# Kernel tuning notes

Hardware: AMD Instinct MI355X
Metric: run time of the kernel (lower is better)

## Reference

```python
import jax, jax.numpy as jnp
import numpy as np

H = 12  # num_attention_heads


def setup_inputs() -> dict:
    key = jax.random.key(0)
    ks = jax.random.split(key, 7)
    B, T, L, D = 4, 64, 128, 768
    input_ids = jax.random.randint(ks[0], (B, T, L), 0, 30000, dtype=jnp.int32)
    speaker_ids = jax.random.randint(ks[1], (B, T), 0, 8, dtype=jnp.int32)
    token_embeddings = jax.random.normal(ks[2], (B, T, L, D), dtype=jnp.float32)
    edu_embeddings = jax.random.normal(ks[3], (B, T, D), dtype=jnp.float32)
    s = 1.0 / np.sqrt(D)
    Wk = jax.random.normal(ks[4], (D, D), dtype=jnp.float32) * s
    Wv = jax.random.normal(ks[5], (D, D), dtype=jnp.float32) * s
    Wq = jax.random.normal(ks[6], (D, D), dtype=jnp.float32) * s
    return {"input_ids": input_ids, "speaker_ids": speaker_ids,
            "token_embeddings": token_embeddings, "edu_embeddings": edu_embeddings,
            "Wk": Wk, "Wv": Wv, "Wq": Wq}


def reference(input_ids, speaker_ids, token_embeddings, edu_embeddings, Wk, Wv, Wq):
    B, T, L = input_ids.shape
    D = token_embeddings.shape[-1]
    d = D // H
    # per-turn keys/values, split into heads: [B,T,H,d]
    k = (edu_embeddings @ Wk.T).reshape(B, T, H, d)
    v = (edu_embeddings @ Wv.T).reshape(B, T, H, d)
    # per-head outer products k (x) v: [B,T,H,d,d]
    kv = jnp.einsum('bthd,bthe->bthde', k, v)
    # speaker-segmented inclusive prefix sum: M[b,t] = sum_{u<=t, spk[u]==spk[t]} kv[b,u]
    same = speaker_ids[:, None, :] == speaker_ids[:, :, None]        # [B,T(t),T(u)]
    causal = jnp.tril(jnp.ones((T, T), dtype=bool))                  # u <= t (inclusive)
    A = (same & causal).astype(kv.dtype)                             # [B,T,T]
    M = jnp.einsum('btu,buhde->bthde', A, kv)                        # [B,T,H,d,d]
    # token queries attend into their turn's speaker memory matrix
    q = (token_embeddings @ Wq.T).reshape(B, T, L, H, d)
    a = jnp.einsum('btlhd,bthde->btlhe', q, M).reshape(B, T, L, D)
    return token_embeddings + a
```

## Files before the change

### kernel.cpp

```cpp
#include <hip/hip_runtime.h>
#include <hip/hip_bf16.h>

#define NB 4
#define NT 64
#define NL 128
#define ND 768
#define NH 12
#define HD 64

typedef __attribute__((ext_vector_type(8))) short short8;
typedef __attribute__((ext_vector_type(4))) float f32x4;
typedef __attribute__((ext_vector_type(4))) unsigned int u32x4;

typedef __attribute__((address_space(3))) unsigned int lds_u32;
typedef __attribute__((address_space(1))) const unsigned int glob_u32;

static __device__ __forceinline__ unsigned short f2b(float x) {
    __hip_bfloat16 h = __float2bfloat16(x);
    return *reinterpret_cast<unsigned short*>(&h);
}
static __device__ __forceinline__ float b2f(unsigned short u) {
    unsigned int v = ((unsigned int)u) << 16;
    union { unsigned int i; float f; } c; c.i = v; return c.f;
}
static __device__ __forceinline__ void gl2lds16(const void* g, void* l) {
    __builtin_amdgcn_global_load_lds((glob_u32*)g, (lds_u32*)l, 16, 0, 0);
}
static __device__ __forceinline__ unsigned rne2(unsigned lo, unsigned hi) {
    lo += 0x7FFFu + ((lo >> 16) & 1u);
    hi += 0x7FFFu + ((hi >> 16) & 1u);
    return __builtin_amdgcn_perm(hi, lo, 0x07060302u);
}

#define TAIL_WQ4  147456u
#define TAIL_EDU4 196608u
#define TAIL_WK4  344064u
__global__ __launch_bounds__(256) void conv_bf16(
    const float* __restrict__ te, const float* __restrict__ Wq,
    const float* __restrict__ edu, const float* __restrict__ Wk,
    const float* __restrict__ Wv, unsigned short* __restrict__ dst)
{
    const unsigned tid = threadIdx.x;
    if (blockIdx.x < 3072u) {
        const unsigned base = blockIdx.x * 2048u + tid;
        u32x4 a[8];
        #pragma unroll
        for (int i = 0; i < 8; i++) {
            const u32x4* s = (const u32x4*)te + (base + i * 256u);
            a[i] = __builtin_nontemporal_load(s);
        }
        #pragma unroll
        for (int i = 0; i < 8; i++) {
            uint2 o;
            o.x = rne2(a[i].x, a[i].y);
            o.y = rne2(a[i].z, a[i].w);
            *(uint2*)(dst + (size_t)(base + i * 256u) * 4u) = o;
        }
    } else {
        const unsigned base = (blockIdx.x - 3072u) * 2048u + tid;
        u32x4 a[8];
        #pragma unroll
        for (int i = 0; i < 8; i++) {
            unsigned c = base + i * 256u;
            const float* s;
            if (c < TAIL_WQ4)       s = Wq  + (size_t)c * 4u;
            else if (c < TAIL_EDU4) s = edu + (size_t)(c - TAIL_WQ4)  * 4u;
            else if (c < TAIL_WK4)  s = Wk  + (size_t)(c - TAIL_EDU4) * 4u;
            else                    s = Wv  + (size_t)(c - TAIL_WK4)  * 4u;
            a[i] = *(const u32x4*)s;
        }
        unsigned short* d = dst + 25165824u;
        #pragma unroll
        for (int i = 0; i < 8; i++) {
            uint2 o;
            o.x = rne2(a[i].x, a[i].y);
            o.y = rne2(a[i].z, a[i].w);
            *(uint2*)(d + (size_t)(base + i * 256u) * 4u) = o;
        }
    }
}

__global__ __launch_bounds__(256) void kvm(
    const unsigned short* __restrict__ edu_b,
    const unsigned short* __restrict__ wk_b,
    const unsigned short* __restrict__ wv_b,
    const int* __restrict__ spk,
    unsigned short* __restrict__ Mt)
{
    const int h = blockIdx.x, b = blockIdx.y, eh = blockIdx.z;

    __shared__ float bucket[8][32][65];
    __shared__ float k_s[64][68];
    __shared__ float v_s[64][36];
    __shared__ __align__(16) unsigned short stage[10240];
    __shared__ int spk_s[64];
    unsigned short* edu_s = stage;
    unsigned short* wk_s  = stage + 4096;
    unsigned short* wv_s  = stage + 8192;

    const int tid = threadIdx.x, lane = tid & 63, wvx = tid >> 6;
    const int lr = lane & 15, lg = lane >> 4, r8 = lane >> 3, l8 = lane & 7;

    { float* p = &bucket[0][0][0];
      for (int i = tid; i < 8 * 32 * 65; i += 256) p[i] = 0.f; }
    if (tid < 64) spk_s[tid] = spk[b * NT + tid];

    const unsigned short* edub = edu_b + (size_t)(b * 64) * ND;
    const unsigned short* wkb  = wk_b + (size_t)(h * 64) * ND;
    const unsigned short* wvb  = wv_b + (size_t)(h * 64 + eh * 32) * ND;

    f32x4 acc_k[4], acc_v[2];
    #pragma unroll
    for (int i = 0; i < 4; i++) acc_k[i] = (f32x4){0.f, 0.f, 0.f, 0.f};
    #pragma unroll
    for (int i = 0; i < 2; i++) acc_v[i] = (f32x4){0.f, 0.f, 0.f, 0.f};

    const int sswz = ((l8 ^ r8) * 8);

    for (int k0 = 0; k0 < ND; k0 += 64) {
        __syncthreads();
        #pragma unroll
        for (int j = 0; j < 5; j++) {
            const int cid = wvx * 5 + j;
            const unsigned short* gs; unsigned short* ls;
            if (cid < 8)       { gs = edub + (size_t)(cid * 8 + r8) * ND;        ls = edu_s + cid * 512; }
            else if (cid < 16) { gs = wkb  + (size_t)((cid - 8) * 8 + r8) * ND;  ls = wk_s + (cid - 8) * 512; }
            else               { gs = wvb  + (size_t)((cid - 16) * 8 + r8) * ND; ls = wv_s + (cid - 16) * 512; }
            gl2lds16(gs + k0 + sswz, ls);
        }
        __syncthreads();
        #pragma unroll
        for (int k32 = 0; k32 < 2; k32++) {
            const int cx = (((k32 * 4 + lg) ^ (lr & 7)) * 8);
            short8 eb = *(const short8*)&edu_s[(wvx * 16 + lr) * 64 + cx];
            #pragma unroll
            for (int jb = 0; jb < 4; jb++) {
                short8 ak = *(const short8*)&wk_s[(jb * 16 + lr) * 64 + cx];
                acc_k[jb] = __builtin_amdgcn_mfma_f32_16x16x32_bf16(ak, eb, acc_k[jb], 0, 0, 0);
            }
            #pragma unroll
            for (int jb = 0; jb < 2; jb++) {
                short8 av = *(const short8*)&wv_s[(jb * 16 + lr) * 64 + cx];
                acc_v[jb] = __builtin_amdgcn_mfma_f32_16x16x32_bf16(av, eb, acc_v[jb], 0, 0, 0);
            }
        }
    }

    {
        const int t = wvx * 16 + lr;
        #pragma unroll
        for (int jb = 0; jb < 4; jb++) *(f32x4*)&k_s[t][jb * 16 + lg * 4] = acc_k[jb];
        #pragma unroll
        for (int jb = 0; jb < 2; jb++) *(f32x4*)&v_s[t][jb * 16 + lg * 4] = acc_v[jb];
    }
    __syncthreads();

    const int e = tid & 31, dg = tid >> 5;
    for (int t = 0; t < NT; t++) {
        const int s = spk_s[t];
        const float vv = v_s[t][e];
        unsigned short tmp[8];
        #pragma unroll
        for (int jj = 0; jj < 8; jj++) {
            float m = bucket[s][e][dg * 8 + jj] + k_s[t][dg * 8 + jj] * vv;
            bucket[s][e][dg * 8 + jj] = m;
            tmp[jj] = f2b(m);
        }
        unsigned short* mpp = Mt + (((size_t)(b * NT + t) * NH + h) * HD + eh * 32 + e) * HD + dg * 8;
        *(short8*)mpp = *(short8*)tmp;
    }
}

__global__ __launch_bounds__(256, 2) void fused_qm(
    const unsigned short* __restrict__ te_b,
    const unsigned short* __restrict__ wq_b,
    const unsigned short* __restrict__ Mt,
    float* __restrict__ out)
{
    const int orig = blockIdx.x;
    const int id   = (orig & 7) * 192 + (orig >> 3);
    const int hp   = id % 6;
    const int bt   = id / 6;

    __shared__ __align__(16) unsigned short smem[32768];
    unsigned short* te0 = smem;
    unsigned short* te1 = smem + 8192;
    unsigned short* wq0 = smem + 16384;
    unsigned short* wq1 = smem + 24576;
    unsigned short* q_s = smem;

    const int tid  = threadIdx.x;
    const int lane = tid & 63;
    const int wvx  = tid >> 6;
    const int lr   = lane & 15;
    const int lg   = lane >> 4;
    const int wm   = wvx >> 1;
    const int wn   = wvx & 1;
    const int r8   = lane >> 3;
    const int l8   = lane & 7;
    const int sswz = (l8 ^ r8) * 8;

    const unsigned short* teb = te_b + (size_t)bt * NL * ND;
    const unsigned short* wqb = wq_b + (size_t)hp * 128 * ND;

    f32x4 acc[4][4];
    #pragma unroll
    for (int i = 0; i < 4; i++)
        #pragma unroll
        for (int j = 0; j < 4; j++) acc[i][j] = (f32x4){0.f, 0.f, 0.f, 0.f};

    auto STAGE = [&](unsigned short* tebuf, unsigned short* wqbuf, int k0) {
        #pragma unroll
        for (int j = 0; j < 4; j++) {
            const int rbase = wvx * 32 + j * 8;
            gl2lds16(teb + (size_t)(rbase + r8) * ND + k0 + sswz, tebuf + rbase * 64);
            gl2lds16(wqb + (size_t)(rbase + r8) * ND + k0 + sswz, wqbuf + rbase * 64);
        }
    };
    auto COMPUTE = [&](const unsigned short* tes, const unsigned short* wqs) {
        #pragma unroll
        for (int k32 = 0; k32 < 2; k32++) {
            const int cx = (((k32 * 4 + lg) ^ (lr & 7)) * 8);
            short8 af[4], bfv[4];
            #pragma unroll
            for (int tm = 0; tm < 4; tm++)
                af[tm] = *(const short8*)&wqs[(wm * 64 + tm * 16 + lr) * 64 + cx];
            #pragma unroll
            for (int tn = 0; tn < 4; tn++)
                bfv[tn] = *(const short8*)&tes[(wn * 64 + tn * 16 + lr) * 64 + cx];
            #pragma unroll
            for (int tm = 0; tm < 4; tm++)
                #pragma unroll
                for (int tn = 0; tn < 4; tn++)
                    acc[tm][tn] = __builtin_amdgcn_mfma_f32_16x16x32_bf16(
                        af[tm], bfv[tn], acc[tm][tn], 0, 0, 0);
        }
    };

    STAGE(te0, wq0, 0);
    asm volatile("s_waitcnt vmcnt(0)" ::: "memory");
    __builtin_amdgcn_sched_barrier(0);
    __builtin_amdgcn_s_barrier();

    #pragma unroll
    for (int kt = 0; kt < 12; kt += 2) {
        STAGE(te1, wq1, (kt + 1) * 64);
        asm volatile("s_waitcnt vmcnt(8)" ::: "memory");
        __builtin_amdgcn_sched_barrier(0);
        __builtin_amdgcn_s_barrier();
        COMPUTE(te0, wq0);
        asm volatile("s_waitcnt lgkmcnt(0)" ::: "memory");
        __builtin_amdgcn_s_barrier();
        if (kt + 2 < 12) {
            STAGE(te0, wq0, (kt + 2) * 64);
            asm volatile("s_waitcnt vmcnt(8)" ::: "memory");
        } else {
            asm volatile("s_waitcnt vmcnt(0)" ::: "memory");
        }
        __builtin_amdgcn_sched_barrier(0);
        __builtin_amdgcn_s_barrier();
        COMPUTE(te1, wq1);
        asm volatile("s_waitcnt lgkmcnt(0)" ::: "memory");
        __builtin_amdgcn_s_barrier();
    }

    #pragma unroll
    for (int tm = 0; tm < 4; tm++) {
        const int d0 = wm * 64 + tm * 16 + lg * 4;
        #pragma unroll
        for (int tn = 0; tn < 4; tn++) {
            const int ltok = wn * 64 + tn * 16 + lr;
            f32x4 a = acc[tm][tn];
            uint2 w2;
            w2.x = (unsigned)f2b(a.x) | ((unsigned)f2b(a.y) << 16);
            w2.y = (unsigned)f2b(a.z) | ((unsigned)f2b(a.w) << 16);
            *(uint2*)&q_s[ltok * 136 + d0] = w2;
        }
    }

    const int h2 = wvx & 1;
    const int lh = wvx >> 1;
    const unsigned short* mp = Mt + ((size_t)(bt * NH) + hp * 2 + h2) * (HD * HD);
    short8 bfr[8];
    #pragma unroll
    for (int tn = 0; tn < 4; tn++)
        #pragma unroll
        for (int k32 = 0; k32 < 2; k32++)
            bfr[tn * 2 + k32] =
                *(const short8*)&mp[(tn * 16 + lr) * 64 + k32 * 32 + lg * 8];
    __syncthreads();

    f32x4 acc2[4][4];
    #pragma unroll
    for (int i = 0; i < 4; i++)
        #pragma unroll
        for (int j = 0; j < 4; j++) acc2[i][j] = (f32x4){0.f, 0.f, 0.f, 0.f};

    #pragma unroll
    for (int k32 = 0; k32 < 2; k32++) {
        const int ko = k32 * 32 + lg * 8;
        short8 af[4];
        #pragma unroll
        for (int tm = 0; tm < 4; tm++)
            af[tm] = *(const short8*)&q_s[(lh * 64 + tm * 16 + lr) * 136 + h2 * 64 + ko];
        #pragma unroll
        for (int tm = 0; tm < 4; tm++)
            #pragma unroll
            for (int tn = 0; tn < 4; tn++)
                acc2[tm][tn] = __builtin_amdgcn_mfma_f32_16x16x32_bf16(
                    af[tm], bfr[tn * 2 + k32], acc2[tm][tn], 0, 0, 0);
    }

    float* ob = out + (size_t)bt * NL * ND;
    #pragma unroll
    for (int tm = 0; tm < 4; tm++) {
        const int l0 = lh * 64 + tm * 16 + lg * 4;
        #pragma unroll
        for (int tn = 0; tn < 4; tn++) {
            const int cg = hp * 128 + h2 * 64 + tn * 16 + lr;
            f32x4 a = acc2[tm][tn];
            #pragma unroll
            for (int r = 0; r < 4; r++) {
                size_t gi = (size_t)(l0 + r) * ND + cg;
                ob[gi] = b2f(teb[gi]) + a[r];
            }
        }
    }
}

extern "C" void kernel_launch(void* const* d_in, const int* in_sizes, int n_in,
                              void* d_out, int out_size, void* d_ws, size_t ws_size,
                              hipStream_t stream)
{
    const int*   spk = (const int*)d_in[1];
    const float* te  = (const float*)d_in[2];
    const float* edu = (const float*)d_in[3];
    const float* Wk  = (const float*)d_in[4];
    const float* Wv  = (const float*)d_in[5];
    const float* Wq  = (const float*)d_in[6];
    float* out = (float*)d_out;

    unsigned short* bf    = (unsigned short*)d_ws;
    unsigned short* te_bb = bf;
    unsigned short* wq_bb = bf + 25165824u;
    unsigned short* edu_b = bf + 25755648u;
    unsigned short* wk_bb = bf + 25952256u;
    unsigned short* wv_bb = bf + 26542080u;
    unsigned short* Mtbuf = bf + 27131904u;

    conv_bf16<<<3312,            256, 0, stream>>>(te, Wq, edu, Wk, Wv, bf);
    kvm      <<<dim3(NH, NB, 2), 256, 0, stream>>>(edu_b, wk_bb, wv_bb, spk, Mtbuf);
    fused_qm <<<6 * NT * NB,     256, 0, stream>>>(te_bb, wq_bb, Mtbuf, out);
}
```

Before: 112.4 us.

## Merge bf16 conversion and KV-memory kernels into one launch

Folds the bf16 conversion kernel and the kvm kernel into a single prep_all launch. The first 96 blocks build the speaker memory and convert edu, Wk and Wv from fp32 on the fly while loading them into LDS. The remaining blocks convert the token embeddings and Wq. This removes one launch, and the separate bf16 round trip for edu, Wk and Wv, and lets the kvm work overlap with the large conversion. In exchange, every block now reserves about 114KB of shared memory, including the pure-conversion blocks, which cuts their occupancy on the memory-bound path.

```diff
diff --git a/kernel.cpp b/kernel.cpp
--- a/kernel.cpp
+++ b/kernel.cpp
@@ -32,101 +32,101 @@
     return __builtin_amdgcn_perm(hi, lo, 0x07060302u);
 }
 
-#define TAIL_WQ4  147456u
-#define TAIL_EDU4 196608u
-#define TAIL_WK4  344064u
-__global__ __launch_bounds__(256) void conv_bf16(
+__global__ __launch_bounds__(256) void prep_all(
     const float* __restrict__ te, const float* __restrict__ Wq,
     const float* __restrict__ edu, const float* __restrict__ Wk,
-    const float* __restrict__ Wv, unsigned short* __restrict__ dst)
-{
-    const unsigned tid = threadIdx.x;
-    if (blockIdx.x < 3072u) {
-        const unsigned base = blockIdx.x * 2048u + tid;
-        u32x4 a[8];
-        #pragma unroll
-        for (int i = 0; i < 8; i++) {
-            const u32x4* s = (const u32x4*)te + (base + i * 256u);
-            a[i] = __builtin_nontemporal_load(s);
-        }
-        #pragma unroll
-        for (int i = 0; i < 8; i++) {
-            uint2 o;
-            o.x = rne2(a[i].x, a[i].y);
-            o.y = rne2(a[i].z, a[i].w);
-            *(uint2*)(dst + (size_t)(base + i * 256u) * 4u) = o;
-        }
-    } else {
-        const unsigned base = (blockIdx.x - 3072u) * 2048u + tid;
-        u32x4 a[8];
-        #pragma unroll
-        for (int i = 0; i < 8; i++) {
-            unsigned c = base + i * 256u;
-            const float* s;
-            if (c < TAIL_WQ4)       s = Wq  + (size_t)c * 4u;
-            else if (c < TAIL_EDU4) s = edu + (size_t)(c - TAIL_WQ4)  * 4u;
-            else if (c < TAIL_WK4)  s = Wk  + (size_t)(c - TAIL_EDU4) * 4u;
-            else                    s = Wv  + (size_t)(c - TAIL_WK4)  * 4u;
-            a[i] = *(const u32x4*)s;
-        }
-        unsigned short* d = dst + 25165824u;
-        #pragma unroll
-        for (int i = 0; i < 8; i++) {
-            uint2 o;
-            o.x = rne2(a[i].x, a[i].y);
-            o.y = rne2(a[i].z, a[i].w);
-            *(uint2*)(d + (size_t)(base + i * 256u) * 4u) = o;
-        }
-    }
-}
-
-__global__ __launch_bounds__(256) void kvm(
-    const unsigned short* __restrict__ edu_b,
-    const unsigned short* __restrict__ wk_b,
-    const unsigned short* __restrict__ wv_b,
-    const int* __restrict__ spk,
+    const float* __restrict__ Wv, const int* __restrict__ spk,
+    unsigned short* __restrict__ te_b, unsigned short* __restrict__ wq_b,
     unsigned short* __restrict__ Mt)
 {
-    const int h = blockIdx.x, b = blockIdx.y, eh = blockIdx.z;
-
-    __shared__ float bucket[8][32][65];
-    __shared__ float k_s[64][68];
-    __shared__ float v_s[64][36];
-    __shared__ __align__(16) unsigned short stage[10240];
-    __shared__ int spk_s[64];
-    unsigned short* edu_s = stage;
-    unsigned short* wk_s  = stage + 4096;
-    unsigned short* wv_s  = stage + 8192;
-
-    const int tid = threadIdx.x, lane = tid & 63, wvx = tid >> 6;
-    const int lr = lane & 15, lg = lane >> 4, r8 = lane >> 3, l8 = lane & 7;
+    __shared__ __align__(16) unsigned char sm[113920];
+    const int tid = threadIdx.x;
+    const unsigned bid = blockIdx.x;
+
+    if (bid >= 96u) {
+        if (bid < 3168u) {
+            const unsigned base = (bid - 96u) * 2048u + tid;
+            u32x4 a[8];
+            #pragma unroll
+            for (int i = 0; i < 8; i++)
+                a[i] = __builtin_nontemporal_load((const u32x4*)te + base + i * 256u);
+            #pragma unroll
+            for (int i = 0; i < 8; i++) {
+                uint2 o;
+                o.x = rne2(a[i].x, a[i].y);
+                o.y = rne2(a[i].z, a[i].w);
+                *(uint2*)(te_b + (size_t)(base + i * 256u) * 4u) = o;
+            }
+        } else {
+            const unsigned base = (bid - 3168u) * 2048u + tid;
+            u32x4 a[8];
+            #pragma unroll
+            for (int i = 0; i < 8; i++)
+                a[i] = *((const u32x4*)Wq + base + i * 256u);
+            #pragma unroll
+            for (int i = 0; i < 8; i++) {
+                uint2 o;
+                o.x = rne2(a[i].x, a[i].y);
+                o.y = rne2(a[i].z, a[i].w);
+                *(uint2*)(wq_b + (size_t)(base + i * 256u) * 4u) = o;
+            }
+        }
+        return;
+    }
+
+    const int h  = bid % 12;
+    const int b  = (bid / 12) & 3;
+    const int eh = bid / 48;
+
+    float (*bucket)[32][65]  = (float (*)[32][65])(sm);
+    float (*k_s)[68]         = (float (*)[68])(sm + 66560);
+    float (*v_s)[36]         = (float (*)[36])(sm + 83968);
+    unsigned short* edu_s    = (unsigned short*)(sm + 93184);
+    unsigned short* wk_s     = edu_s + 4096;
+    unsigned short* wv_s     = edu_s + 8192;
+    int* spk_s               = (int*)(sm + 113664);
+
+    const int lane = tid & 63, wvx = tid >> 6;
+    const int lr = lane & 15, lg = lane >> 4;
 
     { float* p = &bucket[0][0][0];
       for (int i = tid; i < 8 * 32 * 65; i += 256) p[i] = 0.f; }
     if (tid < 64) spk_s[tid] = spk[b * NT + tid];
 
-    const unsigned short* edub = edu_b + (size_t)(b * 64) * ND;
-    const unsigned short* wkb  = wk_b + (size_t)(h * 64) * ND;
-    const unsigned short* wvb  = wv_b + (size_t)(h * 64 + eh * 32) * ND;
+    const float* eduf = edu + (size_t)(b * 64) * ND;
+    const float* wkf  = Wk  + (size_t)(h * 64) * ND;
+    const float* wvf  = Wv  + (size_t)(h * 64 + eh * 32) * ND;
 
     f32x4 acc_k[4], acc_v[2];
     #pragma unroll
     for (int i = 0; i < 4; i++) acc_k[i] = (f32x4){0.f, 0.f, 0.f, 0.f};
     #pragma unroll
     for (int i = 0; i < 2; i++) acc_v[i] = (f32x4){0.f, 0.f, 0.f, 0.f};
-
-    const int sswz = ((l8 ^ r8) * 8);
 
     for (int k0 = 0; k0 < ND; k0 += 64) {
         __syncthreads();
         #pragma unroll
-        for (int j = 0; j < 5; j++) {
-            const int cid = wvx * 5 + j;
-            const unsigned short* gs; unsigned short* ls;
-            if (cid < 8)       { gs = edub + (size_t)(cid * 8 + r8) * ND;        ls = edu_s + cid * 512; }
-            else if (cid < 16) { gs = wkb  + (size_t)((cid - 8) * 8 + r8) * ND;  ls = wk_s + (cid - 8) * 512; }
-            else               { gs = wvb  + (size_t)((cid - 16) * 8 + r8) * ND; ls = wv_s + (cid - 16) * 512; }
-            gl2lds16(gs + k0 + sswz, ls);
+        for (int i = 0; i < 2; i++) {
+            const int g = tid * 2 + i, row = g >> 3, ch = g & 7;
+            const u32x4* p = (const u32x4*)(eduf + (size_t)row * ND + k0 + ch * 8);
+            u32x4 x = p[0], y = p[1];
+            u32x4 o = { rne2(x.x, x.y), rne2(x.z, x.w), rne2(y.x, y.y), rne2(y.z, y.w) };
+            *(u32x4*)&edu_s[row * 64 + ((ch ^ (row & 7)) * 8)] = o;
+        }
+        #pragma unroll
+        for (int i = 0; i < 2; i++) {
+            const int g = tid * 2 + i, row = g >> 3, ch = g & 7;
+            const u32x4* p = (const u32x4*)(wkf + (size_t)row * ND + k0 + ch * 8);
+            u32x4 x = p[0], y = p[1];
+            u32x4 o = { rne2(x.x, x.y), rne2(x.z, x.w), rne2(y.x, y.y), rne2(y.z, y.w) };
+            *(u32x4*)&wk_s[row * 64 + ((ch ^ (row & 7)) * 8)] = o;
+        }
+        {
+            const int g = tid, row = g >> 3, ch = g & 7;
+            const u32x4* p = (const u32x4*)(wvf + (size_t)row * ND + k0 + ch * 8);
+            u32x4 x = p[0], y = p[1];
+            u32x4 o = { rne2(x.x, x.y), rne2(x.z, x.w), rne2(y.x, y.y), rne2(y.z, y.w) };
+            *(u32x4*)&wv_s[row * 64 + ((ch ^ (row & 7)) * 8)] = o;
         }
         __syncthreads();
         #pragma unroll
@@ -343,12 +343,9 @@
     unsigned short* bf    = (unsigned short*)d_ws;
     unsigned short* te_bb = bf;
     unsigned short* wq_bb = bf + 25165824u;
-    unsigned short* edu_b = bf + 25755648u;
-    unsigned short* wk_bb = bf + 25952256u;
-    unsigned short* wv_bb = bf + 26542080u;
-    unsigned short* Mtbuf = bf + 27131904u;
-
-    conv_bf16<<<3312,            256, 0, stream>>>(te, Wq, edu, Wk, Wv, bf);
-    kvm      <<<dim3(NH, NB, 2), 256, 0, stream>>>(edu_b, wk_bb, wv_bb, spk, Mtbuf);
-    fused_qm <<<6 * NT * NB,     256, 0, stream>>>(te_bb, wq_bb, Mtbuf, out);
-}
+    unsigned short* Mtbuf = bf + 25755648u;
+
+    prep_all<<<3240, 256, 0, stream>>>(te, Wq, edu, Wk, Wv, spk,
+                                       te_bb, wq_bb, Mtbuf);
+    fused_qm<<<6 * NT * NB, 256, 0, stream>>>(te_bb, wq_bb, Mtbuf, out);
+}
```

Result: faster. 101.8 us (-9.5%).
